# Optimization experiments

Measured on AMD Instinct MI355X. Metric: run time of the kernel, lower is better.

## Reference

```python
import jax, jax.numpy as jnp
import numpy as np

BATCH = 4        # opt.batch_size
NPATCH = 4096    # patches per batch element
DIM = 256        # feature dim
MAXC = 5         # self.max_classes
T = 0.07         # opt.nce_T
NEG_FILL = -10.0


def setup_inputs() -> dict:
    key = jax.random.key(0)
    k1, k2, k3 = jax.random.split(key, 3)
    N = BATCH * NPATCH
    features_src = jax.random.normal(k1, (N, DIM), jnp.float32)
    features_tgt = jax.random.normal(k2, (N, DIM), jnp.float32)
    classes = jax.random.randint(k3, (N,), 0, MAXC, dtype=jnp.int32)
    return {"features_src": features_src, "features_tgt": features_tgt, "classes": classes}


def reference(features_src, features_tgt, classes):
    # feat_k = feat_k.detach()
    tgt = jax.lax.stop_gradient(features_tgt)

    # positive logits: per-row dot product, divided by temperature
    pos = jnp.sum(features_src * tgt, axis=-1) / T            # [N]

    src_b = features_src.reshape(BATCH, NPATCH, DIM)
    tgt_b = tgt.reshape(BATCH, NPATCH, DIM)
    cls = classes.reshape(BATCH, NPATCH)

    # full negative logit matrix per batch element
    logits = jnp.einsum('bnd,bmd->bnm', src_b, tgt_b)         # [B, n, n]
    same = cls[:, :, None] == cls[:, None, :]                 # [B, n, n] same-class mask

    # per-class smallest negative logit: min over (row in class c, col not in class c)
    row_min = jnp.min(jnp.where(same, jnp.inf, logits), axis=2)          # [B, n]
    class_eq = cls[:, :, None] == jnp.arange(MAXC)[None, None, :]        # [B, n, C]
    class_min = jnp.min(jnp.where(class_eq, row_min[:, :, None], jnp.inf), axis=1)  # [B, C]
    smallest = jnp.minimum(class_min, NEG_FILL) / T                      # [B, C]
    counts = jnp.sum(class_eq, axis=1)                                   # [B, C]

    # per-row pad value and pad multiplicity (num_pairs_should - num_pairs_is = count_c - 1)
    sm_row = jnp.take_along_axis(smallest, cls, axis=1)                  # [B, n]
    npad = jnp.take_along_axis(counts, cls, axis=1) - 1                  # [B, n]

    # logsumexp over [pos, negatives (other classes only), npad copies of smallest]
    lse_neg = jax.nn.logsumexp(jnp.where(same, -jnp.inf, logits / T), axis=2)  # [B, n]
    pad_term = jnp.where(npad > 0,
                         jnp.log(jnp.maximum(npad, 1).astype(jnp.float32)) + sm_row,
                         -jnp.inf)
    pos_b = pos.reshape(BATCH, NPATCH)
    lse = jax.nn.logsumexp(jnp.stack([pos_b, lse_neg, pad_term], axis=-1), axis=-1)
    loss = lse - pos_b                                                   # CE with label 0

    # match torch ordering: rows concatenated per batch, grouped by class (stable)
    order = jnp.argsort(cls, axis=1)  # jnp.argsort is stable
    return jnp.take_along_axis(loss, order, axis=1).reshape(-1)
```

## Files before the change

### kernel.cpp

```cpp
#include <hip/hip_runtime.h>
#include <cstdint>

#define NBATCH 4
#define NPATCH 4096
#define MAXC   5
#define BM 64
#define BN 64
#define NSPLIT 4
#define SPLITCOLS (NPATCH / NSPLIT)
#define NCIT (SPLITCOLS / BN)
#define SCALE  14.285714285714286f
#define SCALE2 20.609929006188747f
#define LN2F   0.6931471805599453f
#define NEGH  -1.0e38f
#define NEGFILL_T -142.85714285714286f
#define NROWS (NBATCH * NPATCH)

typedef __attribute__((ext_vector_type(8))) short short8;
typedef __attribute__((ext_vector_type(4))) float f32x4;

__device__ __forceinline__ float fexp2(float x) { return __builtin_amdgcn_exp2f(x); }
__device__ __forceinline__ float flog2(float x) { return __builtin_amdgcn_logf(x); }

__device__ __forceinline__ unsigned short f2bf(float f) {
  uint32_t u = __builtin_bit_cast(uint32_t, f);
  u = (u + 0x7FFFu + ((u >> 16) & 1u)) >> 16;
  return (unsigned short)u;
}


__global__ __launch_bounds__(256) void k_aux(const float* __restrict__ src,
                                             const float* __restrict__ tgt,
                                             const int* __restrict__ classes,
                                             unsigned short* __restrict__ tgtb,
                                             unsigned short* __restrict__ srcb,
                                             float* __restrict__ pos,
                                             int* __restrict__ outpos,
                                             int* __restrict__ counts) {
  int blk = blockIdx.x;
  if (blk < 512) {
    int t  = threadIdx.x;
    int tl = blk * 2 + (t >> 7);
    int tt = t & 127;
    int row16 = tt >> 3;
    int kg    = tt & 7;
    size_t rowbase = (size_t)(tl * 16 + row16) * 256 + kg * 32;
    const float4* rs = (const float4*)(src + rowbase);
    const float4* rt_ = (const float4*)(tgt + rowbase);
    uint4* wsrc = (uint4*)srcb + (size_t)tl * 512 + (size_t)(kg * 4) * 16 + row16;
    uint4* wtgt = (uint4*)tgtb + (size_t)tl * 512 + (size_t)(kg * 4) * 16 + row16;
    float d = 0.f;
#pragma unroll
    for (int j = 0; j < 4; ++j) {
      float4 sa = rs[j * 2], sb = rs[j * 2 + 1];
      float4 ta = rt_[j * 2], tb = rt_[j * 2 + 1];
      d += sa.x * ta.x + sa.y * ta.y + sa.z * ta.z + sa.w * ta.w
         + sb.x * tb.x + sb.y * tb.y + sb.z * tb.z + sb.w * tb.w;
      union { ushort4 h[2]; uint4 u; } pk;
      pk.h[0].x = f2bf(sa.x * SCALE2); pk.h[0].y = f2bf(sa.y * SCALE2);
      pk.h[0].z = f2bf(sa.z * SCALE2); pk.h[0].w = f2bf(sa.w * SCALE2);
      pk.h[1].x = f2bf(sb.x * SCALE2); pk.h[1].y = f2bf(sb.y * SCALE2);
      pk.h[1].z = f2bf(sb.z * SCALE2); pk.h[1].w = f2bf(sb.w * SCALE2);
      wsrc[j * 16] = pk.u;
      pk.h[0].x = f2bf(ta.x); pk.h[0].y = f2bf(ta.y);
      pk.h[0].z = f2bf(ta.z); pk.h[0].w = f2bf(ta.w);
      pk.h[1].x = f2bf(tb.x); pk.h[1].y = f2bf(tb.y);
      pk.h[1].z = f2bf(tb.z); pk.h[1].w = f2bf(tb.w);
      wtgt[j * 16] = pk.u;
    }
    d += __shfl_xor(d, 1, 64);
    d += __shfl_xor(d, 2, 64);
    d += __shfl_xor(d, 4, 64);
    if (kg == 0) pos[tl * 16 + row16] = d * SCALE;
    return;
  }

  __shared__ int sa[MAXC * 256];
  __shared__ int sb2[MAXC * 256];
  int b = blk - 512, t = threadIdx.x;
  int base = b * NPATCH + t * 16;
  int cv[16];
#pragma unroll
  for (int e = 0; e < 16; ++e) cv[e] = classes[base + e];
  int cnt[MAXC];
#pragma unroll
  for (int c = 0; c < MAXC; ++c) {
    cnt[c] = 0;
#pragma unroll
    for (int e = 0; e < 16; ++e)
      if (cv[e] == c) cnt[c]++;
  }
#pragma unroll
  for (int c = 0; c < MAXC; ++c) sa[c * 256 + t] = cnt[c];
  __syncthreads();

  int* rp = sa; int* wp = sb2;
  for (int d = 1; d < 256; d <<= 1) {
#pragma unroll
    for (int c = 0; c < MAXC; ++c) {
      int v = rp[c * 256 + t];
      if (t >= d) v += rp[c * 256 + t - d];
      wp[c * 256 + t] = v;
    }
    __syncthreads();
    int* tmp = rp; rp = wp; wp = tmp;
  }

  int tot[MAXC], excl[MAXC], off[MAXC + 1];
  off[0] = 0;
#pragma unroll
  for (int c = 0; c < MAXC; ++c) {
    tot[c]  = rp[c * 256 + 255];
    excl[c] = rp[c * 256 + t] - cnt[c];
    off[c + 1] = off[c] + tot[c];
  }
#pragma unroll
  for (int c = 0; c < MAXC; ++c) {
    int r = off[c] + excl[c];
#pragma unroll
    for (int e = 0; e < 16; ++e)
      if (cv[e] == c) { outpos[base + e] = r; r++; }
  }
  if (t < MAXC) counts[b * MAXC + t] = tot[t];
}

__global__ __launch_bounds__(256) void k_main(const unsigned short* __restrict__ srcb,
                                              const unsigned short* __restrict__ tgtb,
                                              const int* __restrict__ classes,
                                              float* __restrict__ pm,
                                              float* __restrict__ ps) {
  __shared__ float redm[2][BM], reds[2][BM];

  const int blk   = blockIdx.x;
  const int split = blk & (NSPLIT - 1);
  const int rbk   = blk >> 2;
  const int b     = rbk >> 6;
  const int rb    = rbk & 63;
  const int rowstart = b * NPATCH + rb * BM;
  const int tid = threadIdx.x;
  const int w = tid >> 6, lane = tid & 63, q = lane >> 4, l4 = lane & 15;
  const int rh = w >> 1, ch = w & 1;
  const int colbase = b * NPATCH + split * SPLITCOLS;

  const uint4* ap = (const uint4*)srcb + (size_t)(b * 256 + rb * 4 + rh * 2) * 512 + lane;
  uint4 afr[2][8];
#pragma unroll
  for (int rt = 0; rt < 2; ++rt)
#pragma unroll
    for (int ks = 0; ks < 8; ++ks)
      afr[rt][ks] = ap[rt * 512 + ks * 64];

  int rcls[2][4];
#pragma unroll
  for (int rt = 0; rt < 2; ++rt)
#pragma unroll
    for (int r = 0; r < 4; ++r)
      rcls[rt][r] = classes[rowstart + rh * 32 + rt * 16 + q * 4 + r];

  float m_[2][4], s_[2][4];
#pragma unroll
  for (int rt = 0; rt < 2; ++rt)
#pragma unroll
    for (int r = 0; r < 4; ++r) { m_[rt][r] = -INFINITY; s_[rt][r] = 0.f; }

  const uint4* bp = (const uint4*)tgtb
                  + (size_t)(b * 256 + split * 64 + ch * 2) * 512 + lane;
  const int* clp = classes + colbase + ch * 32 + l4;

  uint4 ea0[4], ea1[4], eb0[4], eb1[4];
#define LOADH(d0, d1, uoff)                                                         \
  {                                                                                 \
    _Pragma("unroll")                                                               \
    for (int i = 0; i < 4; ++i) {                                                   \
      d0[i] = bp[(uoff) + i * 64];                                                  \
      d1[i] = bp[(uoff) + i * 64 + 512];                                            \
    }                                                                               \
  }

#define STATS(ac, cc0, cc1)                                                         \
  {                                                                                 \
    _Pragma("unroll")                                                               \
    for (int rt = 0; rt < 2; ++rt) {                                                \
      _Pragma("unroll")                                                             \
      for (int r = 0; r < 4; ++r) {                                                 \
        int rc = rcls[rt][r];                                                       \
        float y0 = ((cc0) == rc) ? NEGH : (ac)[rt][0][r];                           \
        float y1 = ((cc1) == rc) ? NEGH : (ac)[rt][1][r];                           \
        float nm = fmaxf(m_[rt][r], fmaxf(y0, y1));                                 \
        float e01 = fexp2(y0 - nm) + fexp2(y1 - nm);                                \
        s_[rt][r] = fmaf(s_[rt][r], fexp2(m_[rt][r] - nm), e01);                    \
        m_[rt][r] = nm;                                                             \
      }                                                                             \
    }                                                                               \
  }

  LOADH(ea0, ea1, 0);

  const f32x4 zc = {0.f, 0.f, 0.f, 0.f};
  f32x4 pacc[2][2];
  int pc0 = 0, pc1 = 0;

  for (int cit = 0; cit < NCIT; ++cit) {
    f32x4 acc[2][2];

    LOADH(eb0, eb1, cit * 2048 + 256);
    int c0 = clp[cit * 64];
    int c1 = clp[cit * 64 + 16];

#pragma unroll
    for (int ksl = 0; ksl < 4; ++ksl) {
      short8 b0 = __builtin_bit_cast(short8, ea0[ksl]);
      short8 b1 = __builtin_bit_cast(short8, ea1[ksl]);
#pragma unroll
      for (int rt = 0; rt < 2; ++rt) {
        short8 a = __builtin_bit_cast(short8, afr[rt][ksl]);
        acc[rt][0] = __builtin_amdgcn_mfma_f32_16x16x32_bf16(
            a, b0, (ksl == 0) ? zc : acc[rt][0], 0, 0, 0);
        acc[rt][1] = __builtin_amdgcn_mfma_f32_16x16x32_bf16(
            a, b1, (ksl == 0) ? zc : acc[rt][1], 0, 0, 0);
      }
    }

    if (cit + 1 < NCIT) LOADH(ea0, ea1, (cit + 1) * 2048);

    if (cit > 0) STATS(pacc, pc0, pc1);

#pragma unroll
    for (int ksl = 0; ksl < 4; ++ksl) {
      short8 b0 = __builtin_bit_cast(short8, eb0[ksl]);
      short8 b1 = __builtin_bit_cast(short8, eb1[ksl]);
#pragma unroll
      for (int rt = 0; rt < 2; ++rt) {
        short8 a = __builtin_bit_cast(short8, afr[rt][4 + ksl]);
        acc[rt][0] = __builtin_amdgcn_mfma_f32_16x16x32_bf16(a, b0, acc[rt][0], 0, 0, 0);
        acc[rt][1] = __builtin_amdgcn_mfma_f32_16x16x32_bf16(a, b1, acc[rt][1], 0, 0, 0);
      }
    }

#pragma unroll
    for (int rt = 0; rt < 2; ++rt)
#pragma unroll
      for (int ct = 0; ct < 2; ++ct) pacc[rt][ct] = acc[rt][ct];
    pc0 = c0; pc1 = c1;
  }
  STATS(pacc, pc0, pc1);
#undef LOADH
#undef STATS

#pragma unroll
  for (int off = 1; off < 16; off <<= 1) {
#pragma unroll
    for (int rt = 0; rt < 2; ++rt)
#pragma unroll
      for (int r = 0; r < 4; ++r) {
        float om = __shfl_xor(m_[rt][r], off, 64);
        float os = __shfl_xor(s_[rt][r], off, 64);
        float nm = fmaxf(m_[rt][r], om);
        s_[rt][r] = s_[rt][r] * fexp2(m_[rt][r] - nm) + os * fexp2(om - nm);
        m_[rt][r] = nm;
      }
  }

  if (l4 == 0) {
#pragma unroll
    for (int rt = 0; rt < 2; ++rt)
#pragma unroll
      for (int r = 0; r < 4; ++r) {
        int li = rh * 32 + rt * 16 + q * 4 + r;
        redm[ch][li] = m_[rt][r];
        reds[ch][li] = s_[rt][r];
      }
  }
  __syncthreads();
  if (tid < BM) {
    float m0 = redm[0][tid], m1 = redm[1][tid];
    float nm = fmaxf(m0, m1);
    float s  = reds[0][tid] * fexp2(m0 - nm) + reds[1][tid] * fexp2(m1 - nm);
    size_t o = (size_t)split * NROWS + rowstart + tid;
    pm[o] = nm;
    ps[o] = s;
  }
}

__global__ __launch_bounds__(256) void k_fin(const int* __restrict__ classes,
                                             const float* __restrict__ pos,
                                             const float* __restrict__ pm,
                                             const float* __restrict__ ps,
                                             const int* __restrict__ outpos,
                                             const int* __restrict__ counts,
                                             float* __restrict__ out) {
  int n = blockIdx.x * 256 + threadIdx.x;
  int b = n >> 12;
  int c = classes[n];
  float ps_ = pos[n];

  float M2 = -INFINITY;
  float mm[NSPLIT], ss[NSPLIT];
#pragma unroll
  for (int s = 0; s < NSPLIT; ++s) {
    mm[s] = pm[(size_t)s * NROWS + n];
    ss[s] = ps[(size_t)s * NROWS + n];
    M2 = fmaxf(M2, mm[s]);
  }
  float S2 = 0.f;
#pragma unroll
  for (int s = 0; s < NSPLIT; ++s) S2 = fmaf(ss[s], fexp2(mm[s] - M2), S2);
  float ln = (S2 > 0.f) ? (M2 + flog2(S2)) * LN2F : -INFINITY;

  int npad = counts[b * MAXC + c] - 1;
  float pt = (npad > 0) ? (logf((float)npad) + NEGFILL_T) : -INFINITY;
  float M = fmaxf(ps_, fmaxf(ln, pt));
  float lse = M + logf(expf(ps_ - M) + expf(ln - M) + expf(pt - M));
  out[b * NPATCH + outpos[n]] = lse - ps_;
}

extern "C" void kernel_launch(void* const* d_in, const int* in_sizes, int n_in,
                              void* d_out, int out_size, void* d_ws, size_t ws_size,
                              hipStream_t stream) {
  const float* src = (const float*)d_in[0];
  const float* tgt = (const float*)d_in[1];
  const int* cls   = (const int*)d_in[2];
  float* out = (float*)d_out;

  char* ws = (char*)d_ws;
  unsigned short* tgtb = (unsigned short*)(ws);
  unsigned short* srcb = (unsigned short*)(ws + 8388608);
  float* pos    = (float*)(ws + 16777216);
  float* pm     = (float*)(ws + 16842752);
  float* ps     = (float*)(ws + 17104896);
  int*   outpos = (int*)  (ws + 17367040);
  int*   counts = (int*)  (ws + 17432576);

  k_aux<<<512 + NBATCH, 256, 0, stream>>>(src, tgt, cls, tgtb, srcb, pos, outpos, counts);
  k_main<<<NBATCH * (NPATCH / BM) * NSPLIT, 256, 0, stream>>>(srcb, tgtb, cls, pm, ps);
  k_fin<<<NROWS / 256, 256, 0, stream>>>(cls, pos, pm, ps, outpos, counts, out);
}
```

Measured before the change: 131.4 us.

## Use single-wave blocks with 6-way column chunking and XCD-aware block remap

The main kernel now launches one-wave blocks, each owning 32 rows and one of six uneven column chunks, instead of four-wave blocks with a 4-way split and an LDS merge. Blocks are remapped so that consecutive logical blocks land on the same XCD, which improves L2 reuse of the tgt tiles. The shared-memory reduction and __syncthreads are removed, and each wave writes its partial max and sum directly. The finalizer merges six partials instead of four, which adds partial-result traffic in exchange for more, smaller blocks and better load balance.

```diff
diff --git a/kernel.cpp b/kernel.cpp
--- a/kernel.cpp
+++ b/kernel.cpp
@@ -4,11 +4,9 @@
 #define NBATCH 4
 #define NPATCH 4096
 #define MAXC   5
-#define BM 64
-#define BN 64
-#define NSPLIT 4
-#define SPLITCOLS (NPATCH / NSPLIT)
-#define NCIT (SPLITCOLS / BN)
+#define NCHUNK 6
+#define RGROUPS 128
+#define GRID_MAIN (NBATCH * RGROUPS * NCHUNK)
 #define SCALE  14.285714285714286f
 #define SCALE2 20.609929006188747f
 #define LN2F   0.6931471805599453f
@@ -124,25 +122,24 @@
   if (t < MAXC) counts[b * MAXC + t] = tot[t];
 }
 
-__global__ __launch_bounds__(256) void k_main(const unsigned short* __restrict__ srcb,
-                                              const unsigned short* __restrict__ tgtb,
-                                              const int* __restrict__ classes,
-                                              float* __restrict__ pm,
-                                              float* __restrict__ ps) {
-  __shared__ float redm[2][BM], reds[2][BM];
-
-  const int blk   = blockIdx.x;
-  const int split = blk & (NSPLIT - 1);
-  const int rbk   = blk >> 2;
-  const int b     = rbk >> 6;
-  const int rb    = rbk & 63;
-  const int rowstart = b * NPATCH + rb * BM;
-  const int tid = threadIdx.x;
-  const int w = tid >> 6, lane = tid & 63, q = lane >> 4, l4 = lane & 15;
-  const int rh = w >> 1, ch = w & 1;
-  const int colbase = b * NPATCH + split * SPLITCOLS;
-
-  const uint4* ap = (const uint4*)srcb + (size_t)(b * 256 + rb * 4 + rh * 2) * 512 + lane;
+__global__ __launch_bounds__(64) void k_main(const unsigned short* __restrict__ srcb,
+                                             const unsigned short* __restrict__ tgtb,
+                                             const int* __restrict__ classes,
+                                             float* __restrict__ pm,
+                                             float* __restrict__ ps) {
+  const int phys = blockIdx.x;
+  const int lid  = (phys & 7) * (GRID_MAIN / 8) + (phys >> 3);
+  const int b   = lid / (RGROUPS * NCHUNK);
+  const int r2  = lid % (RGROUPS * NCHUNK);
+  const int rg  = r2 / NCHUNK;
+  const int j   = r2 % NCHUNK;
+  const int t0  = (j * 64) / 3;
+  const int t1  = ((j + 1) * 64) / 3;
+  const int lane = threadIdx.x;
+  const int q = lane >> 4, l4 = lane & 15;
+  const int rowstart = b * NPATCH + rg * 32;
+
+  const uint4* ap = (const uint4*)srcb + (size_t)(b * 256 + rg * 2) * 512 + lane;
   uint4 afr[2][8];
 #pragma unroll
   for (int rt = 0; rt < 2; ++rt)
@@ -155,7 +152,7 @@
   for (int rt = 0; rt < 2; ++rt)
 #pragma unroll
     for (int r = 0; r < 4; ++r)
-      rcls[rt][r] = classes[rowstart + rh * 32 + rt * 16 + q * 4 + r];
+      rcls[rt][r] = classes[rowstart + rt * 16 + q * 4 + r];
 
   float m_[2][4], s_[2][4];
 #pragma unroll
@@ -163,9 +160,8 @@
 #pragma unroll
     for (int r = 0; r < 4; ++r) { m_[rt][r] = -INFINITY; s_[rt][r] = 0.f; }
 
-  const uint4* bp = (const uint4*)tgtb
-                  + (size_t)(b * 256 + split * 64 + ch * 2) * 512 + lane;
-  const int* clp = classes + colbase + ch * 32 + l4;
+  const uint4* bp = (const uint4*)tgtb + (size_t)(b * 256 + t0 * 2) * 512 + lane;
+  const int* clp  = classes + b * NPATCH + t0 * 32 + l4;
 
   uint4 ea0[4], ea1[4], eb0[4], eb1[4];
 #define LOADH(d0, d1, uoff)                                                         \
@@ -199,13 +195,14 @@
   const f32x4 zc = {0.f, 0.f, 0.f, 0.f};
   f32x4 pacc[2][2];
   int pc0 = 0, pc1 = 0;
-
-  for (int cit = 0; cit < NCIT; ++cit) {
+  const int nt = t1 - t0;
+
+  for (int it = 0; it < nt; ++it) {
     f32x4 acc[2][2];
 
-    LOADH(eb0, eb1, cit * 2048 + 256);
-    int c0 = clp[cit * 64];
-    int c1 = clp[cit * 64 + 16];
+    LOADH(eb0, eb1, 256);
+    int c0 = clp[0];
+    int c1 = clp[16];
 
 #pragma unroll
     for (int ksl = 0; ksl < 4; ++ksl) {
@@ -221,9 +218,9 @@
       }
     }
 
-    if (cit + 1 < NCIT) LOADH(ea0, ea1, (cit + 1) * 2048);
-
-    if (cit > 0) STATS(pacc, pc0, pc1);
+    if (it + 1 < nt) LOADH(ea0, ea1, 1024);
+
+    if (it > 0) STATS(pacc, pc0, pc1);
 
 #pragma unroll
     for (int ksl = 0; ksl < 4; ++ksl) {
@@ -242,6 +239,8 @@
 #pragma unroll
       for (int ct = 0; ct < 2; ++ct) pacc[rt][ct] = acc[rt][ct];
     pc0 = c0; pc1 = c1;
+    bp  += 1024;
+    clp += 32;
   }
   STATS(pacc, pc0, pc1);
 #undef LOADH
@@ -266,19 +265,10 @@
     for (int rt = 0; rt < 2; ++rt)
 #pragma unroll
       for (int r = 0; r < 4; ++r) {
-        int li = rh * 32 + rt * 16 + q * 4 + r;
-        redm[ch][li] = m_[rt][r];
-        reds[ch][li] = s_[rt][r];
+        size_t o = (size_t)j * NROWS + rowstart + rt * 16 + q * 4 + r;
+        pm[o] = m_[rt][r];
+        ps[o] = s_[rt][r];
       }
-  }
-  __syncthreads();
-  if (tid < BM) {
-    float m0 = redm[0][tid], m1 = redm[1][tid];
-    float nm = fmaxf(m0, m1);
-    float s  = reds[0][tid] * fexp2(m0 - nm) + reds[1][tid] * fexp2(m1 - nm);
-    size_t o = (size_t)split * NROWS + rowstart + tid;
-    pm[o] = nm;
-    ps[o] = s;
   }
 }
 
@@ -295,16 +285,16 @@
   float ps_ = pos[n];
 
   float M2 = -INFINITY;
-  float mm[NSPLIT], ss[NSPLIT];
-#pragma unroll
-  for (int s = 0; s < NSPLIT; ++s) {
+  float mm[NCHUNK], ss[NCHUNK];
+#pragma unroll
+  for (int s = 0; s < NCHUNK; ++s) {
     mm[s] = pm[(size_t)s * NROWS + n];
     ss[s] = ps[(size_t)s * NROWS + n];
     M2 = fmaxf(M2, mm[s]);
   }
   float S2 = 0.f;
 #pragma unroll
-  for (int s = 0; s < NSPLIT; ++s) S2 = fmaf(ss[s], fexp2(mm[s] - M2), S2);
+  for (int s = 0; s < NCHUNK; ++s) S2 = fmaf(ss[s], fexp2(mm[s] - M2), S2);
   float ln = (S2 > 0.f) ? (M2 + flog2(S2)) * LN2F : -INFINITY;
 
   int npad = counts[b * MAXC + c] - 1;
@@ -327,11 +317,11 @@
   unsigned short* srcb = (unsigned short*)(ws + 8388608);
   float* pos    = (float*)(ws + 16777216);
   float* pm     = (float*)(ws + 16842752);
-  float* ps     = (float*)(ws + 17104896);
-  int*   outpos = (int*)  (ws + 17367040);
-  int*   counts = (int*)  (ws + 17432576);
+  float* ps     = (float*)(ws + 17235968);
+  int*   outpos = (int*)  (ws + 17629184);
+  int*   counts = (int*)  (ws + 17694720);
 
   k_aux<<<512 + NBATCH, 256, 0, stream>>>(src, tgt, cls, tgtb, srcb, pos, outpos, counts);
-  k_main<<<NBATCH * (NPATCH / BM) * NSPLIT, 256, 0, stream>>>(srcb, tgtb, cls, pm, ps);
+  k_main<<<GRID_MAIN, 64, 0, stream>>>(srcb, tgtb, cls, pm, ps);
   k_fin<<<NROWS / 256, 256, 0, stream>>>(cls, pos, pm, ps, outpos, counts, out);
 }
```

Result: no change. 131.0 us (-0.3%).
